# Kernel tuning notes

Hardware: AMD Instinct MI355X
Metric: run time of the kernel (lower is better)

Reference implementation:

```python
import jax, jax.numpy as jnp
import numpy as np

M, K, N = 2048, 4096, 11008
Q_ABS_MAX = 128.0  # x_scaled_abs_max_fp for w8a8
Q_MIN, Q_MAX = -128, 127


def setup_inputs() -> dict:
    key = jax.random.key(0)
    k1, k2, k3, k4 = jax.random.split(key, 4)
    x = jax.random.normal(k1, (M, K), dtype=jnp.float32)
    # pre-quantized int8 weight, stored [K, N] (transposed layout as in quantize_weights)
    w_q = jax.random.randint(k2, (K, N), Q_MIN, Q_MAX + 1, dtype=jnp.int32).astype(jnp.int8)
    bias = jax.random.normal(k3, (N,), dtype=jnp.float32) * 0.01
    # per-tensor weight dequant scale (q_scale of the quantized weight)
    y_scale = jax.random.uniform(k4, (1,), dtype=jnp.float32, minval=0.001, maxval=0.02)
    return {"x": x, "w_q": w_q, "bias": bias, "y_scale": y_scale}


def reference(x, w_q, bias, y_scale):
    # dynamic per-tensor activation quantization: scale = max|x| / 128
    x_scale = jnp.max(jnp.abs(x)) / jnp.float32(Q_ABS_MAX)
    x_q = jnp.clip(jnp.round(x / x_scale), Q_MIN, Q_MAX).astype(jnp.int8)
    c = jnp.matmul(x_q.astype(jnp.int32), w_q.astype(jnp.int32))
    # dequantize + bias
    y = c.astype(jnp.float32) * (x_scale * y_scale[0]) + bias
    return y
```

## Files before the change

kernel.cpp:

```cpp
#include <hip/hip_runtime.h>
#include <stdint.h>

#define M_DIM 2048
#define K_DIM 4096
#define N_DIM 11008

typedef int v4i  __attribute__((ext_vector_type(4)));
typedef int v16i __attribute__((ext_vector_type(16)));

#define WS_XQ_OFF   65536ull
#define WS_WT_OFF   8454144ull
#define WS_FULL_BYTES (8454144ull + 45088768ull)
#define WS_SMALL_BYTES 8454144ull

static __device__ __forceinline__ void llds16(const void* g, void* l) {
  __builtin_amdgcn_global_load_lds(
      reinterpret_cast<const uint32_t __attribute__((address_space(1)))*>(
          reinterpret_cast<uintptr_t>(g)),
      reinterpret_cast<uint32_t __attribute__((address_space(3)))*>(
          reinterpret_cast<uintptr_t>(l)),
      16, 0, 0);
}

__global__ __launch_bounds__(256) void absmax_kernel(const float* __restrict__ x,
                                                     float* __restrict__ part) {
  __shared__ float red[256];
  const int g = blockIdx.x * 256 + threadIdx.x;
  const float4* x4 = reinterpret_cast<const float4*>(x);
  float m = 0.f;
#pragma unroll
  for (int i = 0; i < 8; ++i) {
    float4 v = x4[(size_t)i * 262144 + g];
    m = fmaxf(m, fmaxf(fmaxf(fabsf(v.x), fabsf(v.y)),
                       fmaxf(fabsf(v.z), fabsf(v.w))));
  }
  red[threadIdx.x] = m;
  __syncthreads();
  for (int s = 128; s > 0; s >>= 1) {
    if (threadIdx.x < s) red[threadIdx.x] = fmaxf(red[threadIdx.x], red[threadIdx.x + s]);
    __syncthreads();
  }
  if (threadIdx.x == 0) part[blockIdx.x] = red[0];
}

__global__ __launch_bounds__(256) void finalize_scale(const float* __restrict__ part,
                                                      const float* __restrict__ y_scale,
                                                      float* __restrict__ scales) {
  __shared__ float red[256];
  const int t = threadIdx.x;
  float m = fmaxf(fmaxf(part[t], part[t + 256]), fmaxf(part[t + 512], part[t + 768]));
  red[t] = m;
  __syncthreads();
  for (int s = 128; s > 0; s >>= 1) {
    if (t < s) red[t] = fmaxf(red[t], red[t + s]);
    __syncthreads();
  }
  if (t == 0) {
    float xs = red[0] * (1.0f / 128.0f);
    scales[0] = xs;
    scales[1] = xs * y_scale[0];
  }
}

static __device__ __forceinline__ int quant4(float4 v, float s) {
  int q0 = (int)rintf(v.x / s);
  int q1 = (int)rintf(v.y / s);
  int q2 = (int)rintf(v.z / s);
  int q3 = (int)rintf(v.w / s);
  q0 = max(-128, min(127, q0));
  q1 = max(-128, min(127, q1));
  q2 = max(-128, min(127, q2));
  q3 = max(-128, min(127, q3));
  return (q0 & 255) | ((q1 & 255) << 8) | ((q2 & 255) << 16) | ((q3 & 255) << 24);
}

__global__ __launch_bounds__(256) void quant_pack(const float* __restrict__ x,
                                                  const float* __restrict__ scales,
                                                  signed char* __restrict__ xq) {
  const float s = scales[0];
  const int g = blockIdx.x * 256 + threadIdx.x;
  const int mblk = g >> 15;
  const int kt = (g >> 9) & 63;
  const int u = g & 511;
  const int row = mblk * 128 + ((u >> 7) & 3) * 32 + (u & 31);
  const int kf = kt * 64 + ((u >> 6) & 1) * 32 + ((u >> 5) & 1) * 16;
  const float4* xp = reinterpret_cast<const float4*>(x + (size_t)row * K_DIM + kf);
  v4i o;
#pragma unroll
  for (int i = 0; i < 4; ++i) o[i] = quant4(xp[i], s);
  *reinterpret_cast<v4i*>(xq + (size_t)g * 16) = o;
}

__global__ __launch_bounds__(256) void quant_rowmajor(const float* __restrict__ x,
                                                      const float* __restrict__ scales,
                                                      signed char* __restrict__ xq) {
  const float s = scales[0];
  const size_t t = (size_t)blockIdx.x * 256 + threadIdx.x;
  const float4* x4 = reinterpret_cast<const float4*>(x) + t * 4;
  v4i o;
#pragma unroll
  for (int i = 0; i < 4; ++i) o[i] = quant4(x4[i], s);
  *reinterpret_cast<v4i*>(xq + t * 16) = o;
}

__global__ __launch_bounds__(256) void transpose_pack(const int* __restrict__ w,
                                                      signed char* __restrict__ wt) {
  __shared__ int tile[64 * 65];
  const int t = threadIdx.x;
  const int bx = blockIdx.x;
  const int by = blockIdx.y;
  const int n0 = bx * 64;
  const int k0 = by * 64;
#pragma unroll
  for (int p = 0; p < 4; ++p) {
    const int id = p * 256 + t;
    const int r = id >> 4;
    const int c4 = id & 15;
    v4i v = *reinterpret_cast<const v4i*>(w + (size_t)(k0 + r) * N_DIM + n0 + c4 * 4);
    tile[r * 65 + c4 * 4 + 0] = v[0];
    tile[r * 65 + c4 * 4 + 1] = v[1];
    tile[r * 65 + c4 * 4 + 2] = v[2];
    tile[r * 65 + c4 * 4 + 3] = v[3];
  }
  __syncthreads();
  const int nl = ((t >> 7) << 5) | (t & 31);
  const int kc = (t >> 5) & 3;
  v4i o;
#pragma unroll
  for (int q = 0; q < 4; ++q) {
    const int kb = kc * 16 + q * 4;
    int b0 = tile[(kb + 0) * 65 + nl] & 255;
    int b1 = tile[(kb + 1) * 65 + nl] & 255;
    int b2 = tile[(kb + 2) * 65 + nl] & 255;
    int b3 = tile[(kb + 3) * 65 + nl] & 255;
    o[q] = b0 | (b1 << 8) | (b2 << 16) | (b3 << 24);
  }
  const size_t base = ((size_t)(bx >> 2) * 64 + by) * 16384;
  const int ubase = ((bx & 3) * 2) << 7;
  *reinterpret_cast<v4i*>(wt + base + (size_t)(ubase + t) * 16) = o;
}

#define V9_TILE_B 24576
#define V9_NT     (K_DIM / 64)

__global__ __launch_bounds__(256, 2) void gemm_i8_v9(
    const signed char* __restrict__ xq, const signed char* __restrict__ wt,
    const float* __restrict__ scales, const float* __restrict__ bias,
    float* __restrict__ y) {
  __shared__ __align__(16) signed char smem[3 * V9_TILE_B];
  const int tid = threadIdx.x;

  const int bid = blockIdx.x;
  const int swz = (bid & 7) * 86 + (bid >> 3);
  const int mblk = swz & 15;
  const int nblk = swz >> 4;
  const int m0 = mblk * 128;
  const int n0 = nblk * 256;

  const signed char* gA = xq + (size_t)mblk * 64 * 8192;
  const signed char* gB = wt + (size_t)nblk * 64 * 16384;
  signed char* const ld = smem + tid * 16;

#define STAGE(kt, soff)                                                       \
  do {                                                                        \
    const size_t a_ = (size_t)(kt) * 8192 + tid * 16;                         \
    const size_t b_ = (size_t)(kt) * 16384 + tid * 16;                        \
    llds16(gA + a_,         ld + (soff));                                     \
    llds16(gA + a_ + 4096,  ld + (soff) + 4096);                              \
    llds16(gB + b_,         ld + (soff) + 8192);                              \
    llds16(gB + b_ + 4096,  ld + (soff) + 12288);                             \
    llds16(gB + b_ + 8192,  ld + (soff) + 16384);                             \
    llds16(gB + b_ + 12288, ld + (soff) + 20480);                             \
  } while (0)

  const int lane = tid & 63;
  const int wid = tid >> 6;
  const int wm = wid >> 1;
  const int wn = wid & 1;
  const int aoff = (wm * 2) * 2048 + lane * 16;
  const int boff = 8192 + (wn * 4) * 2048 + lane * 16;

  v16i acc[2][4] = {};

#define COMPUTE(roff)                                                          \
  do {                                                                         \
    const signed char* bp_ = smem + (roff);                                    \
    _Pragma("unroll")                                                          \
    for (int ks_ = 0; ks_ < 2; ++ks_) {                                        \
      v4i a0 = *reinterpret_cast<const v4i*>(bp_ + aoff + ks_ * 1024);         \
      v4i a1 = *reinterpret_cast<const v4i*>(bp_ + aoff + 2048 + ks_ * 1024);  \
      v4i b0 = *reinterpret_cast<const v4i*>(bp_ + boff + ks_ * 1024);         \
      v4i b1 = *reinterpret_cast<const v4i*>(bp_ + boff + 2048 + ks_ * 1024);  \
      v4i b2 = *reinterpret_cast<const v4i*>(bp_ + boff + 4096 + ks_ * 1024);  \
      v4i b3 = *reinterpret_cast<const v4i*>(bp_ + boff + 6144 + ks_ * 1024);  \
      acc[0][0] = __builtin_amdgcn_mfma_i32_32x32x32_i8(a0, b0, acc[0][0], 0, 0, 0); \
      acc[0][1] = __builtin_amdgcn_mfma_i32_32x32x32_i8(a0, b1, acc[0][1], 0, 0, 0); \
      acc[0][2] = __builtin_amdgcn_mfma_i32_32x32x32_i8(a0, b2, acc[0][2], 0, 0, 0); \
      acc[0][3] = __builtin_amdgcn_mfma_i32_32x32x32_i8(a0, b3, acc[0][3], 0, 0, 0); \
      acc[1][0] = __builtin_amdgcn_mfma_i32_32x32x32_i8(a1, b0, acc[1][0], 0, 0, 0); \
      acc[1][1] = __builtin_amdgcn_mfma_i32_32x32x32_i8(a1, b1, acc[1][1], 0, 0, 0); \
      acc[1][2] = __builtin_amdgcn_mfma_i32_32x32x32_i8(a1, b2, acc[1][2], 0, 0, 0); \
      acc[1][3] = __builtin_amdgcn_mfma_i32_32x32x32_i8(a1, b3, acc[1][3], 0, 0, 0); \
    }                                                                          \
  } while (0)

  STAGE(0, 0);
  STAGE(1, V9_TILE_B);
  asm volatile("s_waitcnt vmcnt(6)" ::: "memory");
  __builtin_amdgcn_s_barrier();

  int rOff = 0;
  int sOff = 2 * V9_TILE_B;
  for (int t = 0; t < V9_NT - 2; ++t) {
    STAGE(t + 2, sOff);
    COMPUTE(rOff);
    asm volatile("s_waitcnt vmcnt(6)" ::: "memory");
    __builtin_amdgcn_s_barrier();
    rOff = (rOff == 2 * V9_TILE_B) ? 0 : rOff + V9_TILE_B;
    sOff = (sOff == 2 * V9_TILE_B) ? 0 : sOff + V9_TILE_B;
  }
  COMPUTE(rOff);
  asm volatile("s_waitcnt vmcnt(0)" ::: "memory");
  __builtin_amdgcn_s_barrier();
  rOff = (rOff == 2 * V9_TILE_B) ? 0 : rOff + V9_TILE_B;
  COMPUTE(rOff);

#undef STAGE
#undef COMPUTE

  const float s = scales[1];
  const int l31 = lane & 31;
  const int lh4 = (lane >> 5) * 4;
#pragma unroll
  for (int fb = 0; fb < 4; ++fb) {
    const int col = n0 + wn * 128 + fb * 32 + l31;
    const float bv = bias[col];
#pragma unroll
    for (int fa = 0; fa < 2; ++fa) {
      const int rbase = m0 + wm * 64 + fa * 32 + lh4;
#pragma unroll
      for (int reg = 0; reg < 16; ++reg) {
        const int row = rbase + (reg & 3) + 8 * (reg >> 2);
        y[(size_t)row * N_DIM + col] = (float)acc[fa][fb][reg] * s + bv;
      }
    }
  }
}

#if defined(__has_builtin)
#if __has_builtin(__builtin_amdgcn_sdot4)
#define HAVE_SDOT4 1
#endif
#endif

static __device__ __forceinline__ int dot4(int a, int b, int c) {
#ifdef HAVE_SDOT4
  return __builtin_amdgcn_sdot4(a, b, c, false);
#else
  c += (int)(signed char)(a) * (int)(signed char)(b);
  c += (int)(signed char)(a >> 8) * (int)(signed char)(b >> 8);
  c += (int)(signed char)(a >> 16) * (int)(signed char)(b >> 16);
  c += (int)(signed char)(a >> 24) * (int)(signed char)(b >> 24);
  return c;
#endif
}

__global__ __launch_bounds__(256) void gemm_fallback(
    const signed char* __restrict__ xq, const int* __restrict__ w,
    const float* __restrict__ scales, const float* __restrict__ bias,
    float* __restrict__ y) {
  __shared__ int lds_a[64 * 17];
  __shared__ int lds_b[64 * 17];
  const int t = threadIdx.x;
  const int m0 = blockIdx.y * 64;
  const int n0 = blockIdx.x * 64;
  const int my = (t >> 4) * 4;
  const int nx = (t & 15) * 4;
  int acc[4][4] = {};
  for (int kt = 0; kt < K_DIM / 64; ++kt) {
    const int k0 = kt * 64;
    {
      const int r = t >> 2, sg = t & 3;
      v4i v = *reinterpret_cast<const v4i*>(xq + (size_t)(m0 + r) * K_DIM + k0 + sg * 16);
      lds_a[r * 17 + sg * 4 + 0] = v[0];
      lds_a[r * 17 + sg * 4 + 1] = v[1];
      lds_a[r * 17 + sg * 4 + 2] = v[2];
      lds_a[r * 17 + sg * 4 + 3] = v[3];
    }
    {
      const int n = t & 63, bkk = (t >> 6) * 4;
#pragma unroll
      for (int q = 0; q < 4; ++q) {
        const int kk = bkk + q;
        int b0 = w[(size_t)(k0 + kk * 4 + 0) * N_DIM + n0 + n] & 255;
        int b1 = w[(size_t)(k0 + kk * 4 + 1) * N_DIM + n0 + n] & 255;
        int b2 = w[(size_t)(k0 + kk * 4 + 2) * N_DIM + n0 + n] & 255;
        int b3 = w[(size_t)(k0 + kk * 4 + 3) * N_DIM + n0 + n] & 255;
        lds_b[n * 17 + kk] = b0 | (b1 << 8) | (b2 << 16) | (b3 << 24);
      }
    }
    __syncthreads();
#pragma unroll
    for (int kk = 0; kk < 16; ++kk) {
      int a[4], b[4];
#pragma unroll
      for (int i = 0; i < 4; ++i) a[i] = lds_a[(my + i) * 17 + kk];
#pragma unroll
      for (int j = 0; j < 4; ++j) b[j] = lds_b[(nx + j) * 17 + kk];
#pragma unroll
      for (int i = 0; i < 4; ++i)
#pragma unroll
        for (int j = 0; j < 4; ++j) acc[i][j] = dot4(a[i], b[j], acc[i][j]);
    }
    __syncthreads();
  }
  const float s = scales[1];
#pragma unroll
  for (int i = 0; i < 4; ++i)
#pragma unroll
    for (int j = 0; j < 4; ++j)
      y[(size_t)(m0 + my + i) * N_DIM + n0 + nx + j] =
          (float)acc[i][j] * s + bias[n0 + nx + j];
}

extern "C" void kernel_launch(void* const* d_in, const int* in_sizes, int n_in,
                              void* d_out, int out_size, void* d_ws, size_t ws_size,
                              hipStream_t stream) {
  (void)in_sizes; (void)n_in; (void)out_size;
  const float* x = (const float*)d_in[0];
  const int* w = (const int*)d_in[1];
  const float* bias = (const float*)d_in[2];
  const float* yscale = (const float*)d_in[3];
  float* y = (float*)d_out;
  char* ws = (char*)d_ws;
  float* scales = (float*)(ws);
  float* part = (float*)(ws + 1024);
  signed char* xq = (signed char*)(ws + WS_XQ_OFF);
  signed char* wt = (signed char*)(ws + WS_WT_OFF);

  if (ws_size < WS_SMALL_BYTES) return;

  absmax_kernel<<<1024, 256, 0, stream>>>(x, part);
  finalize_scale<<<1, 256, 0, stream>>>(part, yscale, scales);
  if (ws_size >= WS_FULL_BYTES) {
    quant_pack<<<2048, 256, 0, stream>>>(x, scales, xq);
    transpose_pack<<<dim3(N_DIM / 64, K_DIM / 64), 256, 0, stream>>>(w, wt);
    gemm_i8_v9<<<(M_DIM / 128) * (N_DIM / 256), 256, 0, stream>>>(xq, wt, scales, bias, y);
  } else {
    quant_rowmajor<<<2048, 256, 0, stream>>>(x, scales, xq);
    gemm_fallback<<<dim3(N_DIM / 64, M_DIM / 64), 256, 0, stream>>>(xq, w, scales, bias, y);
  }
}
```

Measured before the change: 160.9 us.

## Switch GEMM to double-buffered LDS to fit three blocks per CU

Cuts the GEMM's shared-memory pipeline from three stages to two (48KB instead of 72KB) and raises the launch-bounds occupancy hint from 2 to 3 blocks per CU. The main loop is unrolled by two with fixed buffer offsets and waits for all loads to finish before each barrier. The aim is to hide memory latency through more resident blocks rather than deeper prefetch. In exchange, prefetch depth drops to one tile and the occupancy hint limits registers per thread, which could cause spills with the 8 accumulator tiles.

Measured after the change: 176.1 us. 1.09x slower.

```diff
diff --git a/kernel.cpp b/kernel.cpp
--- a/kernel.cpp
+++ b/kernel.cpp
@@ -140,14 +140,14 @@
   *reinterpret_cast<v4i*>(wt + base + (size_t)(ubase + t) * 16) = o;
 }
 
-#define V9_TILE_B 24576
-#define V9_NT     (K_DIM / 64)
-
-__global__ __launch_bounds__(256, 2) void gemm_i8_v9(
+#define V13_TILE_B 24576
+#define V13_NT     (K_DIM / 64)
+
+__global__ __launch_bounds__(256, 3) void gemm_i8_v13(
     const signed char* __restrict__ xq, const signed char* __restrict__ wt,
     const float* __restrict__ scales, const float* __restrict__ bias,
     float* __restrict__ y) {
-  __shared__ __align__(16) signed char smem[3 * V9_TILE_B];
+  __shared__ __align__(16) signed char smem[2 * V13_TILE_B];
   const int tid = threadIdx.x;
 
   const int bid = blockIdx.x;
@@ -205,25 +205,24 @@
   } while (0)
 
   STAGE(0, 0);
-  STAGE(1, V9_TILE_B);
-  asm volatile("s_waitcnt vmcnt(6)" ::: "memory");
-  __builtin_amdgcn_s_barrier();
-
-  int rOff = 0;
-  int sOff = 2 * V9_TILE_B;
-  for (int t = 0; t < V9_NT - 2; ++t) {
-    STAGE(t + 2, sOff);
-    COMPUTE(rOff);
-    asm volatile("s_waitcnt vmcnt(6)" ::: "memory");
-    __builtin_amdgcn_s_barrier();
-    rOff = (rOff == 2 * V9_TILE_B) ? 0 : rOff + V9_TILE_B;
-    sOff = (sOff == 2 * V9_TILE_B) ? 0 : sOff + V9_TILE_B;
-  }
-  COMPUTE(rOff);
   asm volatile("s_waitcnt vmcnt(0)" ::: "memory");
   __builtin_amdgcn_s_barrier();
-  rOff = (rOff == 2 * V9_TILE_B) ? 0 : rOff + V9_TILE_B;
-  COMPUTE(rOff);
+
+  for (int t = 0; t < V13_NT - 2; t += 2) {
+    STAGE(t + 1, V13_TILE_B);
+    COMPUTE(0);
+    asm volatile("s_waitcnt vmcnt(0)" ::: "memory");
+    __builtin_amdgcn_s_barrier();
+    STAGE(t + 2, 0);
+    COMPUTE(V13_TILE_B);
+    asm volatile("s_waitcnt vmcnt(0)" ::: "memory");
+    __builtin_amdgcn_s_barrier();
+  }
+  STAGE(V13_NT - 1, V13_TILE_B);
+  COMPUTE(0);
+  asm volatile("s_waitcnt vmcnt(0)" ::: "memory");
+  __builtin_amdgcn_s_barrier();
+  COMPUTE(V13_TILE_B);
 
 #undef STAGE
 #undef COMPUTE
@@ -345,7 +344,7 @@
   if (ws_size >= WS_FULL_BYTES) {
     quant_pack<<<2048, 256, 0, stream>>>(x, scales, xq);
     transpose_pack<<<dim3(N_DIM / 64, K_DIM / 64), 256, 0, stream>>>(w, wt);
-    gemm_i8_v9<<<(M_DIM / 128) * (N_DIM / 256), 256, 0, stream>>>(xq, wt, scales, bias, y);
+    gemm_i8_v13<<<(M_DIM / 128) * (N_DIM / 256), 256, 0, stream>>>(xq, wt, scales, bias, y);
   } else {
     quant_rowmajor<<<2048, 256, 0, stream>>>(x, scales, xq);
     gemm_fallback<<<dim3(N_DIM / 64, M_DIM / 64), 256, 0, stream>>>(xq, w, scales, bias, y);
```
